# Optimization experiments

Hardware: AMD Instinct MI355X
Metric: run time of the kernel (lower is better)

## Reference

```python
import jax, jax.numpy as jnp
import numpy as np

S = 64.0   # scale (default s)
M = 0.5    # angular margin (default m)
EPS = 1e-07
N, D, C = 2048, 128, 100000

def setup_inputs() -> dict:
    key = jax.random.key(0)
    kx, kw, kl = jax.random.split(key, 3)
    x = jax.random.normal(kx, (N, D), dtype=jnp.float32)
    # NOTE: the torch module never actually normalizes W (local rebinding bug),
    # so W is a raw linear weight. Small init keeps exp(s*wf) finite.
    W = jax.random.normal(kw, (C, D), dtype=jnp.float32) * 0.01
    labels = jax.random.randint(kl, (N,), 0, C, dtype=jnp.int64)
    return {"x": x, "W": W, "labels": labels}

def reference(x, W, labels):
    # L2-normalize embeddings only (matches original: weight normalize is a no-op)
    x_n = x / jnp.linalg.norm(x, axis=1, keepdims=True)
    wf = jnp.einsum('nd,cd->nc', x_n, W)                      # [N, C] logits
    tgt = jnp.take_along_axis(wf, labels[:, None], axis=1)[:, 0]  # wf[i, y_i]
    tgt = jnp.clip(tgt, -1.0 + EPS, 1.0 - EPS)
    numerator = S * jnp.cos(jnp.arccos(tgt) + M)              # margin logit
    # sum over j != y_i of exp(s * wf_ij)
    exp_all = jnp.exp(S * wf)
    excl_sum = jnp.sum(exp_all, axis=1) - jnp.take_along_axis(exp_all, labels[:, None], axis=1)[:, 0]
    denominator = jnp.exp(numerator) + excl_sum
    L = numerator - jnp.log(denominator)
    return -jnp.mean(L)
```

## Files before the change

kernel.cpp:

```cpp
#include <hip/hip_runtime.h>
#include <math.h>

typedef __attribute__((ext_vector_type(8))) short s16x8;
typedef __attribute__((ext_vector_type(4))) float f32x4;

#define N_ROWS 2048
#define D_DIM  128
#define N_CLS  100000
#define N_TILES 782
#define N_PAD   96.0f
#define S_SCALE 64.0f
#define S_LOG2E 92.33248261689366f
#define EPS_F   1e-7f
#define COS_M   0.8775825618903728f
#define SIN_M   0.479425538604203f

#if __has_builtin(__builtin_amdgcn_exp2f)
#define EXP2F(x) __builtin_amdgcn_exp2f(x)
#else
#define EXP2F(x) exp2f(x)
#endif

__device__ __forceinline__ unsigned int f2bf1(float f) {
    unsigned int u = __float_as_uint(f);
    return (u + 0x7FFFu + ((u >> 16) & 1u)) >> 16;
}
__device__ __forceinline__ unsigned int f2bf2(float lo, float hi) {
    return f2bf1(lo) | (f2bf1(hi) << 16);
}

__global__ __launch_bounds__(256)
void k_normalize(const float* __restrict__ x, float* __restrict__ xn,
                 uint4* __restrict__ xb2) {
    const int gt = blockIdx.x;
    const int t = threadIdx.x;
    const int rr = t >> 1, h = t & 1;
    const int row = gt * 128 + rr;

    const f32x4* src = (const f32x4*)(x + (size_t)row * D_DIM + h * 64);
    f32x4 v[16];
    float s = 0.f;
    #pragma unroll
    for (int q = 0; q < 16; q++) {
        v[q] = src[q];
        s += v[q][0]*v[q][0] + v[q][1]*v[q][1] + v[q][2]*v[q][2] + v[q][3]*v[q][3];
    }
    s += __shfl_xor(s, 1);
    const float inv = 1.0f / sqrtf(s);

    f32x4* dxn = (f32x4*)(xn + (size_t)row * D_DIM + h * 64);
    #pragma unroll
    for (int q = 0; q < 16; q++) {
        v[q][0] *= inv; v[q][1] *= inv; v[q][2] *= inv; v[q][3] *= inv;
        dxn[q] = v[q];
    }

    const int wn = rr >> 6, j = (rr >> 4) & 3, lr = rr & 15;
    #pragma unroll
    for (int q2 = 0; q2 < 8; q2++) {
        const int ck = h * 8 + q2;
        const int ks = ck >> 2, lk = ck & 3;
        const int idx = gt * 2048 + wn * 1024 + j * 256 + ks * 64 + lk * 16 + lr;
        f32x4 f0 = v[q2 * 2], f1 = v[q2 * 2 + 1];
        xb2[idx] = make_uint4(f2bf2(f0[0], f0[1]), f2bf2(f0[2], f0[3]),
                              f2bf2(f1[0], f1[1]), f2bf2(f1[2], f1[3]));
    }
}

__global__ __launch_bounds__(256, 3)
void k_main(const uint4* __restrict__ xb2, const float* __restrict__ W,
            float* __restrict__ rowsum) {
    __shared__ uint4 Wsh[2048];
    __shared__ float psum[2][8][128];
    const int t = threadIdx.x;
    const int c0 = blockIdx.y * 128;
    const int half = blockIdx.x;

    #pragma unroll
    for (int m = 0; m < 8; m++) {
        const int idx = m * 256 + t;
        const int lr = idx & 15, lk = (idx >> 4) & 3;
        const int ks = (idx >> 6) & 3, fi = (idx >> 8) & 3, fwm = idx >> 10;
        const int cls = c0 + fwm * 64 + fi * 16 + lr;
        const int k0 = (ks * 4 + lk) * 8;
        uint4 val = make_uint4(0u, 0u, 0u, 0u);
        if (cls < N_CLS) {
            const f32x4* g = (const f32x4*)(W + (size_t)cls * D_DIM + k0);
            f32x4 f0 = g[0], f1 = g[1];
            val.x = f2bf2(f0[0], f0[1]); val.y = f2bf2(f0[2], f0[3]);
            val.z = f2bf2(f1[0], f1[1]); val.w = f2bf2(f1[2], f1[3]);
        }
        Wsh[idx] = val;
    }
    __syncthreads();

    const int lane = t & 63;
    const int wid = t >> 6;
    const int wm = wid >> 1;
    const int wn = wid & 1;
    const int lr = lane & 15;

    for (int it = 0; it < 8; it++) {
        const uint4* bsrc = xb2 + (size_t)(half * 8 + it) * 2048 + wn * 1024;

        uint4 braw[4][4];
        #pragma unroll
        for (int j = 0; j < 4; j++)
            #pragma unroll
            for (int ks = 0; ks < 4; ks++)
                braw[j][ks] = bsrc[j * 256 + ks * 64 + lane];

        f32x4 acc[4][4];
        #pragma unroll
        for (int i = 0; i < 4; i++)
            #pragma unroll
            for (int j = 0; j < 4; j++)
                acc[i][j] = (f32x4){0.f, 0.f, 0.f, 0.f};

        #pragma unroll
        for (int ks = 0; ks < 4; ks++) {
            s16x8 a[4];
            #pragma unroll
            for (int i = 0; i < 4; i++)
                a[i] = *(const s16x8*)&Wsh[wm * 1024 + i * 256 + ks * 64 + lane];
            #pragma unroll
            for (int i = 0; i < 4; i++)
                #pragma unroll
                for (int j = 0; j < 4; j++)
                    acc[i][j] = __builtin_amdgcn_mfma_f32_16x16x32_bf16(
                        a[i], *(const s16x8*)&braw[j][ks], acc[i][j], 0, 0, 0);
        }

        #pragma unroll
        for (int j = 0; j < 4; j++) {
            float pj = 0.f;
            #pragma unroll
            for (int i = 0; i < 4; i++)
                #pragma unroll
                for (int r = 0; r < 4; r++)
                    pj += EXP2F(S_LOG2E * acc[i][j][r]);
            pj += __shfl_xor(pj, 16);
            pj += __shfl_xor(pj, 32);
            if ((lane >> 4) == 0)
                psum[wm][it][wn * 64 + j * 16 + lr] = pj;
        }
    }

    __syncthreads();
    #pragma unroll
    for (int k = 0; k < 4; k++) {
        const int flat = t + k * 256;
        const int it = flat >> 7, r = flat & 127;
        const float v = psum[0][it][r] + psum[1][it][r];
        atomicAdd(&rowsum[half * 1024 + it * 128 + r], v);
    }
}

__global__ void k_tgt(const float* __restrict__ xn, const float* __restrict__ W,
                      const int* __restrict__ labels, float* __restrict__ tgt) {
    int row = blockIdx.x;
    int l = threadIdx.x;
    int y = labels[row];
    const float2* xr = reinterpret_cast<const float2*>(xn + (size_t)row * D_DIM);
    const float2* wr = reinterpret_cast<const float2*>(W + (size_t)y * D_DIM);
    float2 a = xr[l], b = wr[l];
    float s = a.x * b.x + a.y * b.y;
    #pragma unroll
    for (int off = 1; off < 64; off <<= 1) s += __shfl_xor(s, off);
    if (l == 0) tgt[row] = s;
}

__global__ void k_final(const float* __restrict__ rowsum, const float* __restrict__ tgt,
                        float* __restrict__ out) {
    int t = threadIdx.x;
    float lsum = 0.f;
    for (int i = t; i < N_ROWS; i += 256) {
        float tr = tgt[i];
        float tc = fminf(fmaxf(tr, -1.f + EPS_F), 1.f - EPS_F);
        float num = S_SCALE * (tc * COS_M - sqrtf(fmaxf(1.f - tc * tc, 0.f)) * SIN_M);
        float excl = rowsum[i] - N_PAD - __expf(S_SCALE * tr);
        float den = __expf(num) + excl;
        lsum += num - logf(den);
    }
    #pragma unroll
    for (int off = 1; off < 64; off <<= 1) lsum += __shfl_xor(lsum, off);
    __shared__ float wsums[4];
    if ((t & 63) == 0) wsums[t >> 6] = lsum;
    __syncthreads();
    if (t == 0) out[0] = -(wsums[0] + wsums[1] + wsums[2] + wsums[3]) / (float)N_ROWS;
}

extern "C" void kernel_launch(void* const* d_in, const int* in_sizes, int n_in,
                              void* d_out, int out_size, void* d_ws, size_t ws_size,
                              hipStream_t stream) {
    const float* x = (const float*)d_in[0];
    const float* W = (const float*)d_in[1];
    const int* labels = (const int*)d_in[2];
    float* out = (float*)d_out;

    float* xn     = (float*)d_ws;
    uint4* xb2    = (uint4*)(xn + (size_t)N_ROWS * D_DIM);
    float* rowsum = (float*)((char*)xb2 + (size_t)N_ROWS * D_DIM * 2);
    float* tgt    = rowsum + N_ROWS;

    hipMemsetAsync(rowsum, 0, N_ROWS * sizeof(float), stream);
    k_normalize<<<N_ROWS / 128, 256, 0, stream>>>(x, xn, xb2);
    dim3 grid(2, N_TILES);
    k_main<<<grid, 256, 0, stream>>>(xb2, W, rowsum);
    k_tgt<<<N_ROWS, 64, 0, stream>>>(xn, W, labels, tgt);
    k_final<<<1, 256, 0, stream>>>(rowsum, tgt, out);
}
```

Before: 114.7 us.

## Fuse target dot into normalize, single block per class tile, double-buffer B loads

Computes the target logit inside the normalize kernel, which removes the k_tgt launch and the fp32 xn write. k_main now has each block cover all 2048 rows for its 128-class tile, so the W tile is converted to bf16 once per block rather than twice, and the grid is halved. The inner loop is split into per-j phases that prefetch the next B fragment into a ping-pong register buffer, overlapping global loads with MFMA work. Keeping all A fragments in registers raises register pressure, and psum grows, which could reduce occupancy.

```diff
diff --git a/kernel.cpp b/kernel.cpp
--- a/kernel.cpp
+++ b/kernel.cpp
@@ -30,8 +30,9 @@
 }
 
 __global__ __launch_bounds__(256)
-void k_normalize(const float* __restrict__ x, float* __restrict__ xn,
-                 uint4* __restrict__ xb2) {
+void k_normalize(const float* __restrict__ x, const float* __restrict__ W,
+                 const int* __restrict__ labels,
+                 float* __restrict__ tgt, uint4* __restrict__ xb2) {
     const int gt = blockIdx.x;
     const int t = threadIdx.x;
     const int rr = t >> 1, h = t & 1;
@@ -48,11 +49,20 @@
     s += __shfl_xor(s, 1);
     const float inv = 1.0f / sqrtf(s);
 
-    f32x4* dxn = (f32x4*)(xn + (size_t)row * D_DIM + h * 64);
+    const int y = labels[row];
+    const f32x4* wsrc = (const f32x4*)(W + (size_t)y * D_DIM + h * 64);
+    float d = 0.f;
+    #pragma unroll
+    for (int q = 0; q < 16; q++) {
+        f32x4 w = wsrc[q];
+        d += v[q][0]*w[0] + v[q][1]*w[1] + v[q][2]*w[2] + v[q][3]*w[3];
+    }
+    d += __shfl_xor(d, 1);
+    if (h == 0) tgt[row] = d * inv;
+
     #pragma unroll
     for (int q = 0; q < 16; q++) {
         v[q][0] *= inv; v[q][1] *= inv; v[q][2] *= inv; v[q][3] *= inv;
-        dxn[q] = v[q];
     }
 
     const int wn = rr >> 6, j = (rr >> 4) & 3, lr = rr & 15;
@@ -67,21 +77,47 @@
     }
 }
 
+#define PHASE(BCUR, BNEXT, IT, J, ITN, JN, LAST) do {                        \
+    if (!(LAST)) {                                                            \
+        _Pragma("unroll")                                                     \
+        for (int ks_ = 0; ks_ < 4; ks_++)                                     \
+            BNEXT[ks_] = bbase[(ITN) * 2048 + (JN) * 256 + ks_ * 64];         \
+    }                                                                         \
+    f32x4 acc0 = {0.f,0.f,0.f,0.f}, acc1 = {0.f,0.f,0.f,0.f};                 \
+    f32x4 acc2 = {0.f,0.f,0.f,0.f}, acc3 = {0.f,0.f,0.f,0.f};                 \
+    _Pragma("unroll")                                                         \
+    for (int ks_ = 0; ks_ < 4; ks_++) {                                       \
+        const s16x8 b_ = *(const s16x8*)&BCUR[ks_];                           \
+        acc0 = __builtin_amdgcn_mfma_f32_16x16x32_bf16(a_[ks_][0], b_, acc0, 0, 0, 0); \
+        acc1 = __builtin_amdgcn_mfma_f32_16x16x32_bf16(a_[ks_][1], b_, acc1, 0, 0, 0); \
+        acc2 = __builtin_amdgcn_mfma_f32_16x16x32_bf16(a_[ks_][2], b_, acc2, 0, 0, 0); \
+        acc3 = __builtin_amdgcn_mfma_f32_16x16x32_bf16(a_[ks_][3], b_, acc3, 0, 0, 0); \
+    }                                                                         \
+    float pj = 0.f;                                                           \
+    _Pragma("unroll")                                                         \
+    for (int r_ = 0; r_ < 4; r_++)                                            \
+        pj += EXP2F(S_LOG2E * acc0[r_]) + EXP2F(S_LOG2E * acc1[r_])           \
+            + EXP2F(S_LOG2E * acc2[r_]) + EXP2F(S_LOG2E * acc3[r_]);          \
+    pj += __shfl_xor(pj, 16);                                                 \
+    pj += __shfl_xor(pj, 32);                                                 \
+    if ((lane >> 4) == 0)                                                     \
+        psum[wm][IT][wn * 64 + (J) * 16 + lr] = pj;                           \
+} while (0)
+
 __global__ __launch_bounds__(256, 3)
 void k_main(const uint4* __restrict__ xb2, const float* __restrict__ W,
             float* __restrict__ rowsum) {
     __shared__ uint4 Wsh[2048];
-    __shared__ float psum[2][8][128];
+    __shared__ float psum[2][16][128];
     const int t = threadIdx.x;
-    const int c0 = blockIdx.y * 128;
-    const int half = blockIdx.x;
+    const int c0 = blockIdx.x * 128;
 
     #pragma unroll
     for (int m = 0; m < 8; m++) {
         const int idx = m * 256 + t;
-        const int lr = idx & 15, lk = (idx >> 4) & 3;
+        const int flr = idx & 15, lk = (idx >> 4) & 3;
         const int ks = (idx >> 6) & 3, fi = (idx >> 8) & 3, fwm = idx >> 10;
-        const int cls = c0 + fwm * 64 + fi * 16 + lr;
+        const int cls = c0 + fwm * 64 + fi * 16 + flr;
         const int k0 = (ks * 4 + lk) * 8;
         uint4 val = make_uint4(0u, 0u, 0u, 0u);
         if (cls < N_CLS) {
@@ -99,75 +135,33 @@
     const int wm = wid >> 1;
     const int wn = wid & 1;
     const int lr = lane & 15;
-
-    for (int it = 0; it < 8; it++) {
-        const uint4* bsrc = xb2 + (size_t)(half * 8 + it) * 2048 + wn * 1024;
-
-        uint4 braw[4][4];
+    const uint4* bbase = xb2 + wn * 1024 + lane;
+
+    uint4 bA[4], bB[4];
+    s16x8 a_[4][4];
+
+    #pragma unroll
+    for (int ks = 0; ks < 4; ks++) bA[ks] = bbase[ks * 64];
+
+    for (int it = 0; it < 16; it++) {
         #pragma unroll
-        for (int j = 0; j < 4; j++)
-            #pragma unroll
-            for (int ks = 0; ks < 4; ks++)
-                braw[j][ks] = bsrc[j * 256 + ks * 64 + lane];
-
-        f32x4 acc[4][4];
-        #pragma unroll
-        for (int i = 0; i < 4; i++)
-            #pragma unroll
-            for (int j = 0; j < 4; j++)
-                acc[i][j] = (f32x4){0.f, 0.f, 0.f, 0.f};
-
-        #pragma unroll
-        for (int ks = 0; ks < 4; ks++) {
-            s16x8 a[4];
+        for (int ks = 0; ks < 4; ks++)
             #pragma unroll
             for (int i = 0; i < 4; i++)
-                a[i] = *(const s16x8*)&Wsh[wm * 1024 + i * 256 + ks * 64 + lane];
-            #pragma unroll
-            for (int i = 0; i < 4; i++)
-                #pragma unroll
-                for (int j = 0; j < 4; j++)
-                    acc[i][j] = __builtin_amdgcn_mfma_f32_16x16x32_bf16(
-                        a[i], *(const s16x8*)&braw[j][ks], acc[i][j], 0, 0, 0);
-        }
-
-        #pragma unroll
-        for (int j = 0; j < 4; j++) {
-            float pj = 0.f;
-            #pragma unroll
-            for (int i = 0; i < 4; i++)
-                #pragma unroll
-                for (int r = 0; r < 4; r++)
-                    pj += EXP2F(S_LOG2E * acc[i][j][r]);
-            pj += __shfl_xor(pj, 16);
-            pj += __shfl_xor(pj, 32);
-            if ((lane >> 4) == 0)
-                psum[wm][it][wn * 64 + j * 16 + lr] = pj;
-        }
+                a_[ks][i] = *(const s16x8*)&Wsh[wm * 1024 + i * 256 + ks * 64 + lane];
+        PHASE(bA, bB, it, 0, it, 1, false);
+        PHASE(bB, bA, it, 1, it, 2, false);
+        PHASE(bA, bB, it, 2, it, 3, false);
+        PHASE(bB, bA, it, 3, it + 1, 0, it == 15);
     }
 
     __syncthreads();
     #pragma unroll
-    for (int k = 0; k < 4; k++) {
+    for (int k = 0; k < 8; k++) {
         const int flat = t + k * 256;
         const int it = flat >> 7, r = flat & 127;
-        const float v = psum[0][it][r] + psum[1][it][r];
-        atomicAdd(&rowsum[half * 1024 + it * 128 + r], v);
-    }
-}
-
-__global__ void k_tgt(const float* __restrict__ xn, const float* __restrict__ W,
-                      const int* __restrict__ labels, float* __restrict__ tgt) {
-    int row = blockIdx.x;
-    int l = threadIdx.x;
-    int y = labels[row];
-    const float2* xr = reinterpret_cast<const float2*>(xn + (size_t)row * D_DIM);
-    const float2* wr = reinterpret_cast<const float2*>(W + (size_t)y * D_DIM);
-    float2 a = xr[l], b = wr[l];
-    float s = a.x * b.x + a.y * b.y;
-    #pragma unroll
-    for (int off = 1; off < 64; off <<= 1) s += __shfl_xor(s, off);
-    if (l == 0) tgt[row] = s;
+        atomicAdd(&rowsum[it * 128 + r], psum[0][it][r] + psum[1][it][r]);
+    }
 }
 
 __global__ void k_final(const float* __restrict__ rowsum, const float* __restrict__ tgt,
@@ -198,15 +192,12 @@
     const int* labels = (const int*)d_in[2];
     float* out = (float*)d_out;
 
-    float* xn     = (float*)d_ws;
-    uint4* xb2    = (uint4*)(xn + (size_t)N_ROWS * D_DIM);
+    uint4* xb2    = (uint4*)d_ws;
     float* rowsum = (float*)((char*)xb2 + (size_t)N_ROWS * D_DIM * 2);
     float* tgt    = rowsum + N_ROWS;
 
     hipMemsetAsync(rowsum, 0, N_ROWS * sizeof(float), stream);
-    k_normalize<<<N_ROWS / 128, 256, 0, stream>>>(x, xn, xb2);
-    dim3 grid(2, N_TILES);
-    k_main<<<grid, 256, 0, stream>>>(xb2, W, rowsum);
-    k_tgt<<<N_ROWS, 64, 0, stream>>>(xn, W, labels, tgt);
+    k_normalize<<<N_ROWS / 128, 256, 0, stream>>>(x, W, labels, tgt, xb2);
+    k_main<<<N_TILES, 256, 0, stream>>>(xb2, W, rowsum);
     k_final<<<1, 256, 0, stream>>>(rowsum, tgt, out);
 }
```

New measurement: 93.13 us. 1.23x faster.
